# Performance work log

Hardware: AMD Instinct MI355X
Metric: run time of the kernel (lower is better)

The kernel has to match this reference:

```python
import jax, jax.numpy as jnp
import numpy as np

B, DIM, L = 16, 512, 4096          # batch, hidden, num frames
N_FFT, HOP, WIN = 1024, 256, 1024  # STFT config (padding='same')


def setup_inputs() -> dict:
    key = jax.random.key(0)
    k1, k2, k3 = jax.random.split(key, 3)
    x = jax.random.normal(k1, (B, DIM, L), dtype=jnp.float32)
    # Conv1d(dim, 2*n_fft, kernel_size=1) weight/bias; small scale so exp(mag) stays sane
    W = jax.random.normal(k2, (2 * N_FFT, DIM), dtype=jnp.float32) * 0.02
    b = jax.random.normal(k3, (2 * N_FFT,), dtype=jnp.float32) * 0.02
    return {"x": x, "W": W, "b": b}


def reference(x, W, b):
    # 1x1 conv == channel-mixing GEMM: (B, 2*n_fft, L)
    h = jnp.einsum('bdl,od->bol', x, W) + b[None, :, None]
    mag, p = jnp.split(h, 2, axis=1)            # each (B, n_fft, L)
    mag = jnp.minimum(jnp.exp(mag), 100.0)      # exp then clip(max=100)
    S = mag * jax.lax.complex(jnp.cos(p), jnp.sin(p))
    # torch.fft.irfft(S, n_fft, dim=1): crops freq axis to n_fft//2+1 bins
    frames = jnp.fft.irfft(S, n=N_FFT, axis=1)
    # hann window, periodic=True (torch default)
    window = 0.5 * (1.0 - jnp.cos(2.0 * jnp.pi * jnp.arange(WIN, dtype=jnp.float32) / WIN))
    frames = frames * window[None, :, None]
    T = frames.shape[-1]
    out_len = (T - 1) * HOP + WIN
    idx = jnp.arange(T)[None, :] * HOP + jnp.arange(WIN)[:, None]
    y = jnp.zeros((frames.shape[0], out_len), frames.dtype).at[:, idx].add(frames)
    env = jnp.zeros((out_len,), frames.dtype).at[idx].add(
        jnp.broadcast_to((window * window)[:, None], (WIN, T)))
    pad = (WIN - HOP) // 2                      # 'same' padding trim
    return y[:, pad:out_len - pad] / env[pad:out_len - pad]
```

## Files before the change

kernel.cpp:

```cpp
#include <hip/hip_runtime.h>
#include <cstdint>
#include <cstddef>

#define BATCH  16
#define DIMK   512
#define LEN    4096
#define NFFT   1024
#define HOPS   256
#define PADT   384
#define OUTL   1048576
#define KP2    1056
#define KP2U   528
#define K2     4224

typedef __attribute__((ext_vector_type(8))) short  short8;
typedef __attribute__((ext_vector_type(4))) float  f32x4;

__device__ __forceinline__ unsigned short f2bf(float f) {
    unsigned u = __float_as_uint(f);
    u += 0x7FFFu + ((u >> 16) & 1u);
    return (unsigned short)(u >> 16);
}

__device__ __forceinline__ void gld16(const unsigned short* g, unsigned short* l) {
    __builtin_amdgcn_global_load_lds(
        (const __attribute__((address_space(1))) unsigned int*)(const void*)g,
        (__attribute__((address_space(3))) unsigned int*)(void*)l, 16, 0, 0);
}

__global__ void pack_W(const float* __restrict__ W, const float* __restrict__ bvec,
                       unsigned short* __restrict__ Wb, float* __restrict__ bp) {
    const int r = blockIdx.x;
    const int i = r >> 7, j = r & 127;
    const int src = (j < 64) ? (i * 64 + j) : (1024 + i * 64 + (j - 64));
    for (int c = threadIdx.x; c < DIMK; c += 256)
        Wb[r * DIMK + c] = f2bf(W[src * DIMK + c]);
    if (threadIdx.x == 0) bp[r] = bvec[src];
}

__global__ void transpose_x(const float* __restrict__ x, unsigned short* __restrict__ xT) {
    __shared__ float tile[32][33];
    const int b = blockIdx.z;
    const int l0 = blockIdx.x * 32, d0 = blockIdx.y * 32;
    const int tx = threadIdx.x, ty = threadIdx.y;
#pragma unroll
    for (int i = 0; i < 4; ++i)
        tile[ty + 8 * i][tx] = x[((size_t)b * DIMK + d0 + ty + 8 * i) * LEN + l0 + tx];
    __syncthreads();
#pragma unroll
    for (int i = 0; i < 4; ++i)
        xT[((size_t)b * LEN + l0 + ty + 8 * i) * DIMK + d0 + tx] = f2bf(tile[tx][ty + 8 * i]);
}

__global__ void build_D(unsigned short* __restrict__ D) {
    const int idx = blockIdx.x * 256 + threadIdx.x;
    if (idx >= 256 * K2) return;
    const int srow = idx / K2;
    const int col  = idx - srow * K2;
    const int rseg = col / KP2;
    const int jj   = col - rseg * KP2;
    const int n    = srow + 256 * rseg;
    const int k    = jj >> 1;
    const float wv = 0.5f - 0.5f * __cosf((float)n * (6.283185307179586f / 1024.f));
    float v = 0.f;
    if ((jj & 1) == 0) {
        if (k == 0)        v = wv * (1.f / 1024.f);
        else if (k < 512) {
            const int p = (k * n) & 1023;
            v = 2.f * __cosf((float)p * (6.283185307179586f / 1024.f)) * wv * (1.f / 1024.f);
        } else if (k == 512) v = ((n & 1) ? -wv : wv) * (1.f / 1024.f);
    } else {
        if (k >= 1 && k < 512) {
            const int p = (k * n) & 1023;
            v = -2.f * __sinf((float)p * (6.283185307179586f / 1024.f)) * wv * (1.f / 1024.f);
        }
    }
    D[idx] = f2bf(v);
}

__global__ __launch_bounds__(256)
void gemm1_kernel(const unsigned short* __restrict__ A,
                  const unsigned short* __restrict__ Bm,
                  const float* __restrict__ bp,
                  unsigned* __restrict__ Sout)
{
    __shared__ alignas(16) unsigned short Alds[128 * 32];
    __shared__ alignas(16) unsigned short Blds[128 * 32];

    const int tid  = threadIdx.x;
    const int lane = tid & 63, w = tid >> 6;
    const int quad = lane >> 4, ln = lane & 15;
    const int bx = blockIdx.x, by = blockIdx.y, bz = blockIdx.z;
    const int m0 = by * 128, l0 = bx * 128;

    const int c0 = tid, c1 = tid + 256;
    const unsigned short* Asrc0 = A + (size_t)(m0 + (c0 >> 2)) * DIMK + (c0 & 3) * 8;
    const unsigned short* Asrc1 = A + (size_t)(m0 + (c1 >> 2)) * DIMK + (c1 & 3) * 8;
    const unsigned short* Bsrc0 = Bm + ((size_t)bz * LEN + l0 + (c0 >> 2)) * DIMK + (c0 & 3) * 8;
    const unsigned short* Bsrc1 = Bm + ((size_t)bz * LEN + l0 + (c1 >> 2)) * DIMK + (c1 & 3) * 8;

    f32x4 acc[8][2];
#pragma unroll
    for (int a = 0; a < 8; ++a)
#pragma unroll
        for (int c = 0; c < 2; ++c) acc[a][c] = (f32x4){0.f, 0.f, 0.f, 0.f};

    for (int k0 = 0; k0 < DIMK; k0 += 32) {
        gld16(Asrc0 + k0, &Alds[c0 * 8]);
        gld16(Asrc1 + k0, &Alds[c1 * 8]);
        gld16(Bsrc0 + k0, &Blds[c0 * 8]);
        gld16(Bsrc1 + k0, &Blds[c1 * 8]);
        __syncthreads();

        short8 af[8], bfr[2];
#pragma unroll
        for (int rt = 0; rt < 8; ++rt)
            af[rt] = *(const short8*)&Alds[(16 * rt + ln) * 32 + quad * 8];
#pragma unroll
        for (int ct = 0; ct < 2; ++ct)
            bfr[ct] = *(const short8*)&Blds[(32 * w + 16 * ct + ln) * 32 + quad * 8];
#pragma unroll
        for (int rt = 0; rt < 8; ++rt)
#pragma unroll
            for (int ct = 0; ct < 2; ++ct)
                acc[rt][ct] = __builtin_amdgcn_mfma_f32_16x16x32_bf16(af[rt], bfr[ct], acc[rt][ct], 0, 0, 0);
        __syncthreads();
    }

    const int kbase = m0 >> 1;
#pragma unroll
    for (int rt = 0; rt < 4; ++rt) {
#pragma unroll
        for (int reg = 0; reg < 4; ++reg) {
            const int rloc = 16 * rt + quad * 4 + reg;
            const int k = kbase + rloc;
            if (k >= KP2U) continue;
            const float bm  = bp[m0 + rloc];
            const float bph = bp[m0 + 64 + rloc];
#pragma unroll
            for (int ct = 0; ct < 2; ++ct) {
                const int l = l0 + 32 * w + 16 * ct + ln;
                const float hm = acc[rt][ct][reg] + bm;
                const float hp = acc[rt + 4][ct][reg] + bph;
                const float mag = fminf(__expf(hm), 100.0f);
                const float re = mag * __cosf(hp);
                const float im = mag * __sinf(hp);
                Sout[((size_t)bz * LEN + l) * KP2U + k] =
                    (unsigned)f2bf(re) | ((unsigned)f2bf(im) << 16);
            }
        }
    }
}

__device__ __forceinline__ float env_at(int q, int s) {
    if (q >= 3 && q <= 4095) return 1.5f;
    float env = 0.f;
#pragma unroll
    for (int r = 0; r < 4; ++r) {
        const int t = q - r;
        if (t >= 0 && t < LEN) {
            const float w = 0.5f - 0.5f * __cosf((float)(s + 256 * r) * (6.283185307179586f / 1024.f));
            env += w * w;
        }
    }
    return env;
}

__global__ __launch_bounds__(256)
void gemm2_kernel(const unsigned short* __restrict__ D,
                  const unsigned short* __restrict__ Sm,
                  float* __restrict__ yout)
{
    __shared__ alignas(16) unsigned short Alds[4 * 128 * 32];
    __shared__ alignas(16) unsigned short Blds[132 * 32];

    const int tid  = threadIdx.x;
    const int lane = tid & 63, w = tid >> 6;
    const int quad = lane >> 4, ln = lane & 15;
    const int sh = w >> 1, qh = w & 1;
    const int bx = blockIdx.x, by = blockIdx.y, bz = blockIdx.z;
    const int qt0 = bx * 128, s0 = by * 128;

    const size_t srowbase = (size_t)bz * LEN;

    f32x4 acc[4][4];
#pragma unroll
    for (int a = 0; a < 4; ++a)
#pragma unroll
        for (int c = 0; c < 4; ++c) acc[a][c] = (f32x4){0.f, 0.f, 0.f, 0.f};

    for (int kk = 0; kk < KP2; kk += 32) {
#pragma unroll
        for (int i = 0; i < 8; ++i) {
            const int ca = i * 256 + tid;
            const int rseg = ca >> 9, rem = ca & 511;
            const int row = rem >> 2, cq = rem & 3;
            gld16(D + (size_t)(s0 + row) * K2 + rseg * KP2 + kk + cq * 8,
                  &Alds[ca * 8]);
        }
        {
            const int cb0 = tid, cb1 = tid + 256;
            const int r0 = cb0 >> 2, q0 = cb0 & 3, le0 = qt0 + r0 - 2;
            const int r1 = cb1 >> 2, q1 = cb1 & 3, le1 = qt0 + r1 - 2;
            uint4 v0 = {0, 0, 0, 0}, v1 = {0, 0, 0, 0};
            if ((unsigned)le0 < (unsigned)LEN)
                v0 = *(const uint4*)&Sm[(srowbase + le0) * KP2 + kk + q0 * 8];
            if ((unsigned)le1 < (unsigned)LEN)
                v1 = *(const uint4*)&Sm[(srowbase + le1) * KP2 + kk + q1 * 8];
            *(uint4*)&Blds[cb0 * 8] = v0;
            *(uint4*)&Blds[cb1 * 8] = v1;
            if (tid < 16) {
                const int cb2 = 512 + tid;
                const int r2 = cb2 >> 2, q2 = cb2 & 3, le2 = qt0 + r2 - 2;
                uint4 v2 = {0, 0, 0, 0};
                if ((unsigned)le2 < (unsigned)LEN)
                    v2 = *(const uint4*)&Sm[(srowbase + le2) * KP2 + kk + q2 * 8];
                *(uint4*)&Blds[cb2 * 8] = v2;
            }
        }
        __syncthreads();

#pragma unroll
        for (int rseg = 0; rseg < 4; ++rseg) {
            short8 af[4], bfr[4];
#pragma unroll
            for (int rt = 0; rt < 4; ++rt)
                af[rt] = *(const short8*)&Alds[rseg * 4096 + (64 * sh + 16 * rt + ln) * 32 + quad * 8];
#pragma unroll
            for (int ct = 0; ct < 4; ++ct)
                bfr[ct] = *(const short8*)&Blds[(3 - rseg + 64 * qh + 16 * ct + ln) * 32 + quad * 8];
#pragma unroll
            for (int rt = 0; rt < 4; ++rt)
#pragma unroll
                for (int ct = 0; ct < 4; ++ct)
                    acc[rt][ct] = __builtin_amdgcn_mfma_f32_16x16x32_bf16(af[rt], bfr[ct], acc[rt][ct], 0, 0, 0);
        }
        __syncthreads();
    }

    float* yb = yout + (size_t)bz * OUTL;
#pragma unroll
    for (int rt = 0; rt < 4; ++rt)
#pragma unroll
        for (int ct = 0; ct < 4; ++ct) {
            const int qi = qt0 + 64 * qh + 16 * ct + ln;
            const int q  = qi + 1;
#pragma unroll
            for (int reg = 0; reg < 4; ++reg) {
                const int s = s0 + 64 * sh + 16 * rt + quad * 4 + reg;
                const int j = 256 * qi + s - 128;
                if ((unsigned)j < (unsigned)OUTL)
                    yb[j] = acc[rt][ct][reg] / env_at(q, s);
            }
        }
}

extern "C" void kernel_launch(void* const* d_in, const int* in_sizes, int n_in,
                              void* d_out, int out_size, void* d_ws, size_t ws_size,
                              hipStream_t stream) {
    const float* x    = (const float*)d_in[0];
    const float* W    = (const float*)d_in[1];
    const float* bvec = (const float*)d_in[2];
    float* y = (float*)d_out;
    char* ws = (char*)d_ws;

    unsigned short* xT = (unsigned short*)(ws);
    unsigned short* Wb = (unsigned short*)(ws + 67108864);
    float*          bp = (float*)(ws + 68288512);
    unsigned short* D  = (unsigned short*)(ws + 68293120);
    unsigned*       S  = (unsigned*)(ws + 70455808);

    transpose_x<<<dim3(128, 16, BATCH), dim3(32, 8), 0, stream>>>(x, xT);
    pack_W<<<dim3(1152), dim3(256), 0, stream>>>(W, bvec, Wb, bp);
    build_D<<<dim3((256 * K2 + 255) / 256), dim3(256), 0, stream>>>(D);

    gemm1_kernel<<<dim3(32, 9, BATCH), dim3(256), 0, stream>>>(Wb, xT, bp, S);

    gemm2_kernel<<<dim3(33, 2, BATCH), dim3(256), 0, stream>>>(
        D, (const unsigned short*)S, y);
}
```

Measured before the change: 592.6 us.

## Stage GEMM epilogues through LDS for coalesced stores and double-buffer D tiles

gemm1 now loops over three M-tiles per block, so each block reuses its x tile location, and writes S through an LDS staging buffer as 16-byte coalesced rows instead of scattered 4-byte stores. gemm2 replaces the single 4-segment A tile with a two-slot double buffer that prefetches the next segment while computing the current one, which cuts LDS use. Its epilogue also goes through LDS, so each thread writes f32x4 vectors and uses a multiply by 2/3 in the steady-state region. The cost is extra barriers per segment and epilogue pass, and fewer gemm1 blocks in flight.

```diff
diff --git a/kernel.cpp b/kernel.cpp
--- a/kernel.cpp
+++ b/kernel.cpp
@@ -84,76 +84,91 @@
                   const float* __restrict__ bp,
                   unsigned* __restrict__ Sout)
 {
-    __shared__ alignas(16) unsigned short Alds[128 * 32];
-    __shared__ alignas(16) unsigned short Blds[128 * 32];
+    __shared__ alignas(16) char smem[17408];
+    unsigned short* Alds = (unsigned short*)smem;
+    unsigned short* Blds = (unsigned short*)(smem + 8192);
+    unsigned*       epi  = (unsigned*)smem;
 
     const int tid  = threadIdx.x;
     const int lane = tid & 63, w = tid >> 6;
     const int quad = lane >> 4, ln = lane & 15;
     const int bx = blockIdx.x, by = blockIdx.y, bz = blockIdx.z;
-    const int m0 = by * 128, l0 = bx * 128;
+    const int l0 = bx * 128;
 
     const int c0 = tid, c1 = tid + 256;
-    const unsigned short* Asrc0 = A + (size_t)(m0 + (c0 >> 2)) * DIMK + (c0 & 3) * 8;
-    const unsigned short* Asrc1 = A + (size_t)(m0 + (c1 >> 2)) * DIMK + (c1 & 3) * 8;
     const unsigned short* Bsrc0 = Bm + ((size_t)bz * LEN + l0 + (c0 >> 2)) * DIMK + (c0 & 3) * 8;
     const unsigned short* Bsrc1 = Bm + ((size_t)bz * LEN + l0 + (c1 >> 2)) * DIMK + (c1 & 3) * 8;
 
-    f32x4 acc[8][2];
-#pragma unroll
-    for (int a = 0; a < 8; ++a)
-#pragma unroll
-        for (int c = 0; c < 2; ++c) acc[a][c] = (f32x4){0.f, 0.f, 0.f, 0.f};
-
-    for (int k0 = 0; k0 < DIMK; k0 += 32) {
-        gld16(Asrc0 + k0, &Alds[c0 * 8]);
-        gld16(Asrc1 + k0, &Alds[c1 * 8]);
-        gld16(Bsrc0 + k0, &Blds[c0 * 8]);
-        gld16(Bsrc1 + k0, &Blds[c1 * 8]);
-        __syncthreads();
-
-        short8 af[8], bfr[2];
-#pragma unroll
-        for (int rt = 0; rt < 8; ++rt)
-            af[rt] = *(const short8*)&Alds[(16 * rt + ln) * 32 + quad * 8];
-#pragma unroll
-        for (int ct = 0; ct < 2; ++ct)
-            bfr[ct] = *(const short8*)&Blds[(32 * w + 16 * ct + ln) * 32 + quad * 8];
-#pragma unroll
-        for (int rt = 0; rt < 8; ++rt)
+    for (int mi = 0; mi < 3; ++mi) {
+        const int mt = by * 3 + mi;
+        const int m0 = mt * 128;
+        const int kbase = mt * 64;
+
+        const unsigned short* Asrc0 = A + (size_t)(m0 + (c0 >> 2)) * DIMK + (c0 & 3) * 8;
+        const unsigned short* Asrc1 = A + (size_t)(m0 + (c1 >> 2)) * DIMK + (c1 & 3) * 8;
+
+        f32x4 acc[8][2];
+#pragma unroll
+        for (int a = 0; a < 8; ++a)
+#pragma unroll
+            for (int c = 0; c < 2; ++c) acc[a][c] = (f32x4){0.f, 0.f, 0.f, 0.f};
+
+        for (int k0 = 0; k0 < DIMK; k0 += 32) {
+            gld16(Asrc0 + k0, &Alds[c0 * 8]);
+            gld16(Asrc1 + k0, &Alds[c1 * 8]);
+            gld16(Bsrc0 + k0, &Blds[c0 * 8]);
+            gld16(Bsrc1 + k0, &Blds[c1 * 8]);
+            __syncthreads();
+
+            short8 af[8], bfr[2];
+#pragma unroll
+            for (int rt = 0; rt < 8; ++rt)
+                af[rt] = *(const short8*)&Alds[((16 * rt + ln) * 4 + quad) * 8];
 #pragma unroll
             for (int ct = 0; ct < 2; ++ct)
-                acc[rt][ct] = __builtin_amdgcn_mfma_f32_16x16x32_bf16(af[rt], bfr[ct], acc[rt][ct], 0, 0, 0);
-        __syncthreads();
-    }
-
-    const int kbase = m0 >> 1;
-#pragma unroll
-    for (int rt = 0; rt < 4; ++rt) {
-#pragma unroll
-        for (int reg = 0; reg < 4; ++reg) {
-            const int rloc = 16 * rt + quad * 4 + reg;
-            const int k = kbase + rloc;
-            if (k >= KP2U) continue;
-            const float bm  = bp[m0 + rloc];
-            const float bph = bp[m0 + 64 + rloc];
-#pragma unroll
-            for (int ct = 0; ct < 2; ++ct) {
-                const int l = l0 + 32 * w + 16 * ct + ln;
-                const float hm = acc[rt][ct][reg] + bm;
-                const float hp = acc[rt + 4][ct][reg] + bph;
-                const float mag = fminf(__expf(hm), 100.0f);
-                const float re = mag * __cosf(hp);
-                const float im = mag * __sinf(hp);
-                Sout[((size_t)bz * LEN + l) * KP2U + k] =
-                    (unsigned)f2bf(re) | ((unsigned)f2bf(im) << 16);
-            }
+                bfr[ct] = *(const short8*)&Blds[((32 * w + 16 * ct + ln) * 4 + quad) * 8];
+#pragma unroll
+            for (int rt = 0; rt < 8; ++rt)
+#pragma unroll
+                for (int ct = 0; ct < 2; ++ct)
+                    acc[rt][ct] = __builtin_amdgcn_mfma_f32_16x16x32_bf16(af[rt], bfr[ct], acc[rt][ct], 0, 0, 0);
+            __syncthreads();
+        }
+
+#pragma unroll
+        for (int ct = 0; ct < 2; ++ct) {
+            const int lrow = w * 16 + ln;
+#pragma unroll
+            for (int rt = 0; rt < 4; ++rt) {
+                unsigned pk[4];
+#pragma unroll
+                for (int reg = 0; reg < 4; ++reg) {
+                    const int rloc = 16 * rt + quad * 4 + reg;
+                    const float hm = acc[rt][ct][reg]     + bp[m0 + rloc];
+                    const float hp = acc[rt + 4][ct][reg] + bp[m0 + 64 + rloc];
+                    const float mag = fminf(__expf(hm), 100.0f);
+                    pk[reg] = (unsigned)f2bf(mag * __cosf(hp)) |
+                              ((unsigned)f2bf(mag * __sinf(hp)) << 16);
+                }
+                *(uint4*)&epi[lrow * 68 + 16 * rt + 4 * quad] = *(uint4*)pk;
+            }
+            __syncthreads();
+#pragma unroll
+            for (int i = 0; i < 4; ++i) {
+                const int c = i * 256 + tid;
+                const int row = c >> 4, kc = c & 15;
+                if (kbase + kc * 4 < KP2U) {
+                    const int l = l0 + 32 * (row >> 4) + 16 * ct + (row & 15);
+                    uint4 v = *(const uint4*)&epi[row * 68 + kc * 4];
+                    *(uint4*)&Sout[((size_t)bz * LEN + l) * KP2U + kbase + kc * 4] = v;
+                }
+            }
+            __syncthreads();
         }
     }
 }
 
 __device__ __forceinline__ float env_at(int q, int s) {
-    if (q >= 3 && q <= 4095) return 1.5f;
     float env = 0.f;
 #pragma unroll
     for (int r = 0; r < 4; ++r) {
@@ -171,8 +186,10 @@
                   const unsigned short* __restrict__ Sm,
                   float* __restrict__ yout)
 {
-    __shared__ alignas(16) unsigned short Alds[4 * 128 * 32];
-    __shared__ alignas(16) unsigned short Blds[132 * 32];
+    __shared__ alignas(16) char smem[24832];
+    unsigned short* Albuf = (unsigned short*)smem;
+    unsigned short* Blds  = (unsigned short*)(smem + 16384);
+    float*          epi   = (float*)smem;
 
     const int tid  = threadIdx.x;
     const int lane = tid & 63, w = tid >> 6;
@@ -182,6 +199,7 @@
     const int qt0 = bx * 128, s0 = by * 128;
 
     const size_t srowbase = (size_t)bz * LEN;
+    const int ca0 = tid, ca1 = tid + 256;
 
     f32x4 acc[4][4];
 #pragma unroll
@@ -190,69 +208,84 @@
         for (int c = 0; c < 4; ++c) acc[a][c] = (f32x4){0.f, 0.f, 0.f, 0.f};
 
     for (int kk = 0; kk < KP2; kk += 32) {
-#pragma unroll
-        for (int i = 0; i < 8; ++i) {
-            const int ca = i * 256 + tid;
-            const int rseg = ca >> 9, rem = ca & 511;
-            const int row = rem >> 2, cq = rem & 3;
-            gld16(D + (size_t)(s0 + row) * K2 + rseg * KP2 + kk + cq * 8,
-                  &Alds[ca * 8]);
-        }
         {
-            const int cb0 = tid, cb1 = tid + 256;
-            const int r0 = cb0 >> 2, q0 = cb0 & 3, le0 = qt0 + r0 - 2;
-            const int r1 = cb1 >> 2, q1 = cb1 & 3, le1 = qt0 + r1 - 2;
+            const int r0 = ca0 >> 2, q0 = ca0 & 3, le0 = qt0 + r0 - 2;
+            const int r1 = ca1 >> 2, q1 = ca1 & 3, le1 = qt0 + r1 - 2;
             uint4 v0 = {0, 0, 0, 0}, v1 = {0, 0, 0, 0};
             if ((unsigned)le0 < (unsigned)LEN)
                 v0 = *(const uint4*)&Sm[(srowbase + le0) * KP2 + kk + q0 * 8];
             if ((unsigned)le1 < (unsigned)LEN)
                 v1 = *(const uint4*)&Sm[(srowbase + le1) * KP2 + kk + q1 * 8];
-            *(uint4*)&Blds[cb0 * 8] = v0;
-            *(uint4*)&Blds[cb1 * 8] = v1;
+            *(uint4*)&Blds[ca0 * 8] = v0;
+            *(uint4*)&Blds[ca1 * 8] = v1;
             if (tid < 16) {
-                const int cb2 = 512 + tid;
-                const int r2 = cb2 >> 2, q2 = cb2 & 3, le2 = qt0 + r2 - 2;
+                const int c2 = 512 + tid;
+                const int r2 = c2 >> 2, q2 = c2 & 3, le2 = qt0 + r2 - 2;
                 uint4 v2 = {0, 0, 0, 0};
                 if ((unsigned)le2 < (unsigned)LEN)
                     v2 = *(const uint4*)&Sm[(srowbase + le2) * KP2 + kk + q2 * 8];
-                *(uint4*)&Blds[cb2 * 8] = v2;
-            }
-        }
+                *(uint4*)&Blds[c2 * 8] = v2;
+            }
+        }
+        gld16(D + (size_t)(s0 + (ca0 >> 2)) * K2 + kk + (ca0 & 3) * 8, &Albuf[ca0 * 8]);
+        gld16(D + (size_t)(s0 + (ca1 >> 2)) * K2 + kk + (ca1 & 3) * 8, &Albuf[ca1 * 8]);
         __syncthreads();
 
 #pragma unroll
         for (int rseg = 0; rseg < 4; ++rseg) {
+            const int buf = rseg & 1;
+            if (rseg < 3) {
+                const unsigned short* src = D + (rseg + 1) * KP2 + kk;
+                gld16(src + (size_t)(s0 + (ca0 >> 2)) * K2 + (ca0 & 3) * 8,
+                      &Albuf[(buf ^ 1) * 4096 + ca0 * 8]);
+                gld16(src + (size_t)(s0 + (ca1 >> 2)) * K2 + (ca1 & 3) * 8,
+                      &Albuf[(buf ^ 1) * 4096 + ca1 * 8]);
+            }
             short8 af[4], bfr[4];
 #pragma unroll
             for (int rt = 0; rt < 4; ++rt)
-                af[rt] = *(const short8*)&Alds[rseg * 4096 + (64 * sh + 16 * rt + ln) * 32 + quad * 8];
+                af[rt] = *(const short8*)&Albuf[buf * 4096 + ((64 * sh + 16 * rt + ln) * 4 + quad) * 8];
 #pragma unroll
             for (int ct = 0; ct < 4; ++ct)
-                bfr[ct] = *(const short8*)&Blds[(3 - rseg + 64 * qh + 16 * ct + ln) * 32 + quad * 8];
+                bfr[ct] = *(const short8*)&Blds[((3 - rseg + 64 * qh + 16 * ct + ln) * 4 + quad) * 8];
 #pragma unroll
             for (int rt = 0; rt < 4; ++rt)
 #pragma unroll
                 for (int ct = 0; ct < 4; ++ct)
                     acc[rt][ct] = __builtin_amdgcn_mfma_f32_16x16x32_bf16(af[rt], bfr[ct], acc[rt][ct], 0, 0, 0);
-        }
+            __syncthreads();
+        }
+    }
+
+    float* yb = yout + (size_t)bz * OUTL;
+#pragma unroll
+    for (int ct = 0; ct < 4; ++ct) {
+        const int qrow = qh * 16 + ln;
+#pragma unroll
+        for (int rt = 0; rt < 4; ++rt)
+            *(f32x4*)&epi[qrow * 132 + 64 * sh + 16 * rt + 4 * quad] = acc[rt][ct];
         __syncthreads();
-    }
-
-    float* yb = yout + (size_t)bz * OUTL;
-#pragma unroll
-    for (int rt = 0; rt < 4; ++rt)
-#pragma unroll
-        for (int ct = 0; ct < 4; ++ct) {
-            const int qi = qt0 + 64 * qh + 16 * ct + ln;
-            const int q  = qi + 1;
-#pragma unroll
-            for (int reg = 0; reg < 4; ++reg) {
-                const int s = s0 + 64 * sh + 16 * rt + quad * 4 + reg;
-                const int j = 256 * qi + s - 128;
-                if ((unsigned)j < (unsigned)OUTL)
-                    yb[j] = acc[rt][ct][reg] / env_at(q, s);
-            }
-        }
+#pragma unroll
+        for (int i = 0; i < 4; ++i) {
+            const int c = i * 256 + tid;
+            const int row = c >> 5, sc = c & 31;
+            const int qi = qt0 + 64 * (row >> 4) + 16 * ct + (row & 15);
+            const int q = qi + 1;
+            const int j = 256 * qi + (s0 + sc * 4) - 128;
+            if ((unsigned)j < (unsigned)(OUTL - 3)) {
+                f32x4 v = *(const f32x4*)&epi[row * 132 + sc * 4];
+                if (q >= 3 && q <= 4095) {
+                    v *= (2.0f / 3.0f);
+                } else {
+#pragma unroll
+                    for (int e = 0; e < 4; ++e)
+                        v[e] /= env_at(q, s0 + sc * 4 + e);
+                }
+                *(f32x4*)&yb[j] = v;
+            }
+        }
+        __syncthreads();
+    }
 }
 
 extern "C" void kernel_launch(void* const* d_in, const int* in_sizes, int n_in,
@@ -274,7 +307,7 @@
     pack_W<<<dim3(1152), dim3(256), 0, stream>>>(W, bvec, Wb, bp);
     build_D<<<dim3((256 * K2 + 255) / 256), dim3(256), 0, stream>>>(D);
 
-    gemm1_kernel<<<dim3(32, 9, BATCH), dim3(256), 0, stream>>>(Wb, xT, bp, S);
+    gemm1_kernel<<<dim3(32, 3, BATCH), dim3(256), 0, stream>>>(Wb, xT, bp, S);
 
     gemm2_kernel<<<dim3(33, 2, BATCH), dim3(256), 0, stream>>>(
         D, (const unsigned short*)S, y);
```

Result: faster. 529.5 us (-10.6%).
